# Kernel tuning notes

Measured on AMD Instinct MI355X. Metric: run time of the kernel, lower is better.

Reference implementation:

```python
import jax, jax.numpy as jnp
import numpy as np

MULTI_SCALE = [1, 3, 7, 9]
H = 8          # attention heads
EPS = 1e-8     # torch F.cosine_similarity eps


def _roi_avg_pool(feats_bct, rois, n_bins):
    """Temporal ROI adaptive average pooling (assumed behavior of `avr(i)`).
    feats_bct: [B, C, T]; rois: [N, 3] int (batch_idx, start, end) -> [N, C, n_bins].
    Bin b covers [s + floor(b*L/n), s + ceil((b+1)*L/n)) like adaptive_avg_pool1d.
    """
    T = feats_bct.shape[2]
    bidx, s, e = rois[:, 0], rois[:, 1], rois[:, 2]
    L = (e - s)[:, None, None]                               # [N,1,1]
    b = jnp.arange(n_bins, dtype=rois.dtype)[None, :, None]  # [1,nb,1]
    t = jnp.arange(T, dtype=rois.dtype)[None, None, :]       # [1,1,T]
    bs = s[:, None, None] + (b * L) // n_bins                # floor
    be = s[:, None, None] - (-(b + 1) * L) // n_bins         # ceil
    mask = ((t >= bs) & (t < be)).astype(feats_bct.dtype)    # [N,nb,T]
    mask = mask / jnp.clip(mask.sum(-1, keepdims=True), 1.0)
    roi_feats = feats_bct[bidx]                              # [N,C,T]
    return jnp.einsum('nit,nct->nci', mask, roi_feats)


def setup_inputs() -> dict:
    key = jax.random.key(0)
    ks = jax.random.split(key, 16)
    B, D, T, N = 4, 1024, 2048, 128
    hec = len(MULTI_SCALE)
    Cg = D // hec  # 256 channels per scale group
    inp = {
        'input_vectors': jax.random.normal(ks[0], (B, D, T), jnp.float32),
        'clstoken_scales': jax.random.normal(ks[1], (B, D), jnp.float32),
    }
    # rois: (batch_idx, start, end) with end > start
    bidx = jax.random.randint(ks[2], (N,), 0, B, jnp.int32)
    s = jax.random.randint(ks[3], (N,), 0, T // 2, jnp.int32)
    length = jax.random.randint(ks[4], (N,), 16, T // 2, jnp.int32)
    inp['rois'] = jnp.stack([bidx, s, jnp.minimum(s + length, T)], axis=1)
    sc = 1.0 / np.sqrt(D)
    inp['Wq'] = jax.random.normal(ks[5], (D, D), jnp.float32) * sc
    inp['bq'] = jnp.zeros((D,), jnp.float32)
    inp['Wk'] = jax.random.normal(ks[6], (D, D), jnp.float32) * sc
    inp['bk'] = jnp.zeros((D,), jnp.float32)
    inp['Wv'] = jax.random.normal(ks[7], (D, D), jnp.float32) * sc
    inp['bv'] = jnp.zeros((D,), jnp.float32)
    for j, nb in enumerate(MULTI_SCALE):
        csc = 1.0 / np.sqrt(Cg * nb)
        inp[f'conv_w{nb}'] = jax.random.normal(ks[8 + j], (Cg, Cg, nb), jnp.float32) * csc
        inp[f'conv_b{nb}'] = jnp.zeros((Cg,), jnp.float32)
    return inp


def reference(input_vectors, clstoken_scales, rois, Wq, bq, Wk, bk, Wv, bv,
              conv_w1, conv_b1, conv_w3, conv_b3, conv_w7, conv_b7, conv_w9, conv_b9):
    B, D, T = input_vectors.shape
    dk = D // H
    hec = len(MULTI_SCALE)
    x = input_vectors.transpose(0, 2, 1)                     # [B,T,D]
    # projections (torch Linear: y = x W^T + b)
    q = clstoken_scales @ Wq.T + bq                          # [B,D]
    k = (x @ Wk.T + bk).reshape(B, T, H, dk).transpose(0, 2, 1, 3)  # [B,H,T,dk]
    v = (x @ Wv.T + bv).reshape(B, T, H, dk).transpose(0, 2, 1, 3)  # [B,H,T,dk]
    qh = q.reshape(B, H, 1, dk)                              # [B,H,1,dk]
    # cosine-similarity pseudo-attention (no repeat blow-up: broadcast instead)
    dot = jnp.einsum('bhqd,bhtd->bht', qh, k)                # [B,H,T]
    nq = jnp.linalg.norm(qh, axis=-1)                        # [B,H,1]
    nk = jnp.linalg.norm(k, axis=-1)                         # [B,H,T]
    cos = dot / jnp.maximum(nq * nk, EPS)
    # eval mode: mask is all-ones, dropout identity
    p_attn = jnp.exp(jnp.abs(cos))                           # [B,H,T]
    val = p_attn[..., None] * v                              # [B,H,T,dk]
    # permute(0,1,3,2).view(B, hec, -1, T): group 2 heads per scale
    val = val.transpose(0, 1, 3, 2).reshape(B, hec, (H // hec) * dk, T)
    conv_ws = [conv_w1, conv_w3, conv_w7, conv_w9]
    conv_bs = [conv_b1, conv_b3, conv_b7, conv_b9]
    outs = []
    for j, nb in enumerate(MULTI_SCALE):
        pooled = _roi_avg_pool(val[:, j], rois, nb)          # [N, D//hec, nb]
        # Conv3d kernel (nb,1,1) stride (nb,1,1) on [N,C,nb,1,1] == full contraction
        outs.append(jnp.einsum('nci,oci->no', pooled, conv_ws[j]) + conv_bs[j])
    return jnp.concatenate(outs, axis=1)                     # [N_roi, D]
```

## Files before the change

kernel.cpp:

```cpp
#include <hip/hip_runtime.h>
#include <hip/hip_bf16.h>
#include <math.h>

#define BB   4
#define DD   1024
#define TT   2048
#define NH   8
#define DKH  128
#define NROI 128

typedef __attribute__((ext_vector_type(8))) __bf16 bf16x8;
typedef __attribute__((ext_vector_type(4))) float  f32x4;

#define OFF_Q    0
#define OFF_NQ   4096
#define OFF_KV   131072
#define OFF_POOL (131072 + 8388608)
#define POOL_FLOATS 655360
#define WS_F32_TOTAL (OFF_POOL + POOL_FLOATS)

__device__ __forceinline__ float bfu2f(unsigned short u) {
    return __uint_as_float(((unsigned int)u) << 16);
}

__global__ __launch_bounds__(256) void qproj_kernel(
    const float* __restrict__ cls, const float* __restrict__ Wq,
    const float* __restrict__ bq, float* __restrict__ q)
{
    const int blk  = blockIdx.x;
    const int b    = blk >> 8;
    const int dg   = blk & 255;
    const int warp = threadIdx.x >> 6;
    const int lane = threadIdx.x & 63;
    const int d    = dg * 4 + warp;
    const float* crow = cls + (size_t)b * DD;
    const float* wrow = Wq + (size_t)d * DD;
    float acc = 0.f;
    for (int i = lane; i < DD; i += 64) acc += crow[i] * wrow[i];
    #pragma unroll
    for (int off = 32; off; off >>= 1) acc += __shfl_down(acc, off);
    if (lane == 0) q[(size_t)b * DD + d] = acc + bq[d];
}

__global__ __launch_bounds__(64) void nq_kernel(
    const float* __restrict__ q, float* __restrict__ nq)
{
    const int bh = blockIdx.x;
    const int lane = threadIdx.x;
    const float* base = q + (size_t)bh * DKH;
    float v0 = base[lane], v1 = base[lane + 64];
    float acc = v0 * v0 + v1 * v1;
    #pragma unroll
    for (int off = 32; off; off >>= 1) acc += __shfl_down(acc, off);
    if (lane == 0) nq[bh] = sqrtf(acc);
}

__global__ __launch_bounds__(256) void convert_pair(
    const float* __restrict__ A, const float* __restrict__ B,
    __hip_bfloat16* __restrict__ Ab, __hip_bfloat16* __restrict__ Bb)
{
    const int i = blockIdx.x * 256 + threadIdx.x;
    float4 a = reinterpret_cast<const float4*>(A)[i];
    float4 b = reinterpret_cast<const float4*>(B)[i];
    union P4 { __hip_bfloat16 h[4]; ushort4 u; } pa, pb;
    pa.h[0] = __float2bfloat16(a.x); pa.h[1] = __float2bfloat16(a.y);
    pa.h[2] = __float2bfloat16(a.z); pa.h[3] = __float2bfloat16(a.w);
    pb.h[0] = __float2bfloat16(b.x); pb.h[1] = __float2bfloat16(b.y);
    pb.h[2] = __float2bfloat16(b.z); pb.h[3] = __float2bfloat16(b.w);
    reinterpret_cast<ushort4*>(Ab)[i] = pa.u;
    reinterpret_cast<ushort4*>(Bb)[i] = pb.u;
}

__global__ __launch_bounds__(256) void transpose_convert(
    const float* __restrict__ X, __hip_bfloat16* __restrict__ Xt)
{
    __shared__ float tile[64][65];
    const int t0 = blockIdx.x * 64, d0 = blockIdx.y * 64, b = blockIdx.z;
    const int tid = threadIdx.x;
    const int g = tid >> 6, tl = tid & 63;
    const float* src = X + ((size_t)(b * DD + d0)) * TT + t0;
    #pragma unroll
    for (int i = 0; i < 16; ++i)
        tile[g * 16 + i][tl] = src[(size_t)(g * 16 + i) * TT + tl];
    __syncthreads();
    const int lane = tid & 63, w = tid >> 6;
    const int dq = (lane & 15) * 4;
    const int th = lane >> 4;
    __hip_bfloat16* dst = Xt + ((size_t)(b * TT + t0)) * DD + d0;
    #pragma unroll
    for (int i = 0; i < 4; ++i) {
        const int t = w * 4 + th + i * 16;
        union { __hip_bfloat16 h[4]; ushort4 u; } P;
        P.h[0] = __float2bfloat16(tile[dq + 0][t]);
        P.h[1] = __float2bfloat16(tile[dq + 1][t]);
        P.h[2] = __float2bfloat16(tile[dq + 2][t]);
        P.h[3] = __float2bfloat16(tile[dq + 3][t]);
        *reinterpret_cast<ushort4*>(&dst[(size_t)t * DD + dq]) = P.u;
    }
}

__device__ __forceinline__ void glds16(const __hip_bfloat16* g, __hip_bfloat16* l)
{
    __builtin_amdgcn_global_load_lds(
        (const __attribute__((address_space(1))) void*)g,
        (__attribute__((address_space(3))) void*)l, 16, 0, 0);
}

__global__ __launch_bounds__(512) void fused_kv(
    const __hip_bfloat16* __restrict__ Wkb,
    const __hip_bfloat16* __restrict__ Wvb,
    const __hip_bfloat16* __restrict__ Xt,
    const float* __restrict__ bk, const float* __restrict__ bv,
    const float* __restrict__ q,  const float* __restrict__ nq,
    __hip_bfloat16* __restrict__ val)
{
    const int t0 = blockIdx.x * 128;
    const int m0 = blockIdx.y * 128;
    const int b  = blockIdx.z;

    __shared__ __hip_bfloat16 AsK[128 * 32];
    __shared__ __hip_bfloat16 AsV[128 * 32];
    __shared__ __hip_bfloat16 Bs[128 * 32];
    __shared__ float qs[128];
    __shared__ float rdot[2][128];
    __shared__ float rsq[2][128];
    __shared__ float p_lds[128];

    const int tid  = threadIdx.x;
    const int lane = tid & 63;
    const int w    = tid >> 6;
    const int wr   = w >> 2;
    const int wc   = w & 3;

    if (tid < 128) qs[tid] = q[(size_t)b * DD + m0 + tid];

    const int st_row = tid >> 2;
    const int st_g   = (tid & 3) ^ ((st_row >> 1) & 3);

    const __hip_bfloat16* WkS = Wkb + (size_t)(m0 + st_row) * DD + st_g * 8;
    const __hip_bfloat16* WvS = Wvb + (size_t)(m0 + st_row) * DD + st_g * 8;
    const __hip_bfloat16* XS  = Xt + ((size_t)(b * TT + t0 + st_row)) * DD + st_g * 8;
    __hip_bfloat16* K0 = AsK + (w * 16) * 32;
    __hip_bfloat16* V0 = AsV + (w * 16) * 32;
    __hip_bfloat16* B0 = Bs  + (w * 16) * 32;

    f32x4 ak[4][2], av[4][2];
    #pragma unroll
    for (int i = 0; i < 4; ++i)
        #pragma unroll
        for (int j = 0; j < 2; ++j) {
            ak[i][j] = (f32x4){0.f, 0.f, 0.f, 0.f};
            av[i][j] = (f32x4){0.f, 0.f, 0.f, 0.f};
        }

    for (int k0 = 0; k0 < DD; k0 += 32) {
        glds16(WkS + k0, K0);
        glds16(WvS + k0, V0);
        glds16(XS  + k0, B0);
        __syncthreads();

        const int g = lane >> 4;
        bf16x8 bfx[2], afk[4], afv[4];
        #pragma unroll
        for (int fn = 0; fn < 2; ++fn) {
            const int r = wc * 32 + fn * 16 + (lane & 15);
            const int s = g ^ ((r >> 1) & 3);
            bfx[fn] = *reinterpret_cast<const bf16x8*>(&Bs[r * 32 + s * 8]);
        }
        #pragma unroll
        for (int fm = 0; fm < 4; ++fm) {
            const int r = wr * 64 + fm * 16 + (lane & 15);
            const int s = g ^ ((r >> 1) & 3);
            afk[fm] = *reinterpret_cast<const bf16x8*>(&AsK[r * 32 + s * 8]);
            afv[fm] = *reinterpret_cast<const bf16x8*>(&AsV[r * 32 + s * 8]);
        }
        #pragma unroll
        for (int fm = 0; fm < 4; ++fm)
            #pragma unroll
            for (int fn = 0; fn < 2; ++fn)
                ak[fm][fn] = __builtin_amdgcn_mfma_f32_16x16x32_bf16(
                    afk[fm], bfx[fn], ak[fm][fn], 0, 0, 0);
        #pragma unroll
        for (int fm = 0; fm < 4; ++fm)
            #pragma unroll
            for (int fn = 0; fn < 2; ++fn)
                av[fm][fn] = __builtin_amdgcn_mfma_f32_16x16x32_bf16(
                    afv[fm], bfx[fn], av[fm][fn], 0, 0, 0);
        __syncthreads();
    }

    const int lg = lane >> 4;
    #pragma unroll
    for (int fn = 0; fn < 2; ++fn) {
        float dp = 0.f, sp = 0.f;
        #pragma unroll
        for (int fm = 0; fm < 4; ++fm) {
            const int mb = wr * 64 + fm * 16 + lg * 4;
            #pragma unroll
            for (int r = 0; r < 4; ++r) {
                const float kv = ak[fm][fn][r] + bk[m0 + mb + r];
                dp += kv * qs[mb + r];
                sp += kv * kv;
            }
        }
        dp += __shfl_xor(dp, 16); sp += __shfl_xor(sp, 16);
        dp += __shfl_xor(dp, 32); sp += __shfl_xor(sp, 32);
        if (lane < 16) {
            rdot[wr][wc * 32 + fn * 16 + lane] = dp;
            rsq[wr][wc * 32 + fn * 16 + lane]  = sp;
        }
    }
    __syncthreads();
    if (tid < 128) {
        const float dd = rdot[0][tid] + rdot[1][tid];
        const float ss = rsq[0][tid] + rsq[1][tid];
        const int head = m0 >> 7;
        const float c = dd / fmaxf(nq[b * NH + head] * sqrtf(ss), 1e-8f);
        p_lds[tid] = expf(fabsf(c));
    }
    __syncthreads();

    float pv[2];
    #pragma unroll
    for (int fn = 0; fn < 2; ++fn)
        pv[fn] = p_lds[wc * 32 + fn * 16 + (lane & 15)];

    const int tbase = t0 + wc * 32 + (lane & 15);
    #pragma unroll
    for (int fm = 0; fm < 4; ++fm) {
        const int m = m0 + wr * 64 + fm * 16 + lg * 4;
        const float4 b4 = *reinterpret_cast<const float4*>(&bv[m]);
        #pragma unroll
        for (int fn = 0; fn < 2; ++fn) {
            const int t = tbase + fn * 16;
            const f32x4 a = av[fm][fn];
            const float pf = pv[fn];
            union { __hip_bfloat16 h[4]; ushort4 u; } P;
            P.h[0] = __float2bfloat16((a[0] + b4.x) * pf);
            P.h[1] = __float2bfloat16((a[1] + b4.y) * pf);
            P.h[2] = __float2bfloat16((a[2] + b4.z) * pf);
            P.h[3] = __float2bfloat16((a[3] + b4.w) * pf);
            *reinterpret_cast<ushort4*>(&val[((size_t)(b * TT + t)) * DD + m]) = P.u;
        }
    }
}

#define POOL_WAVES 16
__global__ __launch_bounds__(1024) void pool_kernel(
    const __hip_bfloat16* __restrict__ val, const int* __restrict__ rois,
    float* __restrict__ pooled)
{
    const int n    = blockIdx.x;
    const int sc   = blockIdx.y;
    const int tid  = threadIdx.x;
    const int lane = tid & 63;
    const int w    = tid >> 6;

    const int nbt[4]  = {1, 3, 7, 9};
    const int offt[4] = {0, 32768, 131072, 360448};
    const int nb  = nbt[sc];
    const int off = offt[sc];

    __shared__ float lacc[9][256];
    for (int i = tid; i < nb * 256; i += 1024)
        ((float*)lacc)[i] = 0.f;

    const int bidx = rois[n * 3 + 0];
    const int s    = rois[n * 3 + 1];
    const int e    = rois[n * 3 + 2];
    const int L    = e - s;
    __syncthreads();

    const int ts = s + (w * L) / POOL_WAVES;
    const int te = s + ((w + 1) * L) / POOL_WAVES;

    const int cq = lane * 4;
    const __hip_bfloat16* vb = val + (size_t)bidx * TT * DD + sc * 256 + cq;

    if (te > ts) {
        int bin = ((ts - s) * nb) / L;
        int nbs = s + ((bin + 1) * L) / nb;
        int cbe = s + ((bin + 1) * L + nb - 1) / nb;

        if (bin > 0 && ts < s + (bin * L + nb - 1) / nb) {
            const ushort4 u = *reinterpret_cast<const ushort4*>(&vb[(size_t)ts * DD]);
            atomicAdd(&lacc[bin - 1][cq + 0], bfu2f(u.x));
            atomicAdd(&lacc[bin - 1][cq + 1], bfu2f(u.y));
            atomicAdd(&lacc[bin - 1][cq + 2], bfu2f(u.z));
            atomicAdd(&lacc[bin - 1][cq + 3], bfu2f(u.w));
        }

        float a0 = 0.f, a1 = 0.f, a2 = 0.f, a3 = 0.f;
        int t = ts;
        while (true) {
            const int seg = min(te, nbs);
            for (; t + 4 <= seg; t += 4) {
                const ushort4 u0 = *reinterpret_cast<const ushort4*>(&vb[(size_t)(t    ) * DD]);
                const ushort4 u1 = *reinterpret_cast<const ushort4*>(&vb[(size_t)(t + 1) * DD]);
                const ushort4 u2 = *reinterpret_cast<const ushort4*>(&vb[(size_t)(t + 2) * DD]);
                const ushort4 u3 = *reinterpret_cast<const ushort4*>(&vb[(size_t)(t + 3) * DD]);
                a0 += bfu2f(u0.x) + bfu2f(u1.x) + bfu2f(u2.x) + bfu2f(u3.x);
                a1 += bfu2f(u0.y) + bfu2f(u1.y) + bfu2f(u2.y) + bfu2f(u3.y);
                a2 += bfu2f(u0.z) + bfu2f(u1.z) + bfu2f(u2.z) + bfu2f(u3.z);
                a3 += bfu2f(u0.w) + bfu2f(u1.w) + bfu2f(u2.w) + bfu2f(u3.w);
            }
            for (; t < seg; ++t) {
                const ushort4 u = *reinterpret_cast<const ushort4*>(&vb[(size_t)t * DD]);
                a0 += bfu2f(u.x); a1 += bfu2f(u.y);
                a2 += bfu2f(u.z); a3 += bfu2f(u.w);
            }
            if (t >= te) break;
            const ushort4 u = *reinterpret_cast<const ushort4*>(&vb[(size_t)t * DD]);
            const float v0 = bfu2f(u.x), v1 = bfu2f(u.y),
                        v2 = bfu2f(u.z), v3 = bfu2f(u.w);
            if (t < cbe) { a0 += v0; a1 += v1; a2 += v2; a3 += v3; }
            atomicAdd(&lacc[bin][cq + 0], a0);
            atomicAdd(&lacc[bin][cq + 1], a1);
            atomicAdd(&lacc[bin][cq + 2], a2);
            atomicAdd(&lacc[bin][cq + 3], a3);
            a0 = v0; a1 = v1; a2 = v2; a3 = v3;
            ++bin; ++t;
            nbs = s + ((bin + 1) * L) / nb;
            cbe = s + ((bin + 1) * L + nb - 1) / nb;
        }
        atomicAdd(&lacc[bin][cq + 0], a0);
        atomicAdd(&lacc[bin][cq + 1], a1);
        atomicAdd(&lacc[bin][cq + 2], a2);
        atomicAdd(&lacc[bin][cq + 3], a3);
    }
    __syncthreads();

    float* po = pooled + off + (size_t)n * 256 * nb;
    for (int i = tid; i < nb * 256; i += 1024) {
        const int bin = i >> 8, ch = i & 255;
        const int bs  = s + (bin * L) / nb;
        const int be  = s + ((bin + 1) * L + nb - 1) / nb;
        po[(size_t)ch * nb + bin] = lacc[bin][ch] / (float)max(be - bs, 1);
    }
}

__global__ __launch_bounds__(256) void out_gemm(
    const float* __restrict__ pooled,
    const float* __restrict__ w1, const float* __restrict__ b1,
    const float* __restrict__ w3, const float* __restrict__ b3,
    const float* __restrict__ w7, const float* __restrict__ b7,
    const float* __restrict__ w9, const float* __restrict__ b9,
    float* __restrict__ out)
{
    const int z = blockIdx.z;
    int sc, kc;
    if      (z == 0)  { sc = 0; kc = 0; }
    else if (z < 4)   { sc = 1; kc = z - 1; }
    else if (z < 11)  { sc = 2; kc = z - 4; }
    else              { sc = 3; kc = z - 11; }

    int nb, off; const float* W; const float* bias;
    switch (sc) {
        case 0:  nb = 1; off = 0;      W = w1; bias = b1; break;
        case 1:  nb = 3; off = 32768;  W = w3; bias = b3; break;
        case 2:  nb = 7; off = 131072; W = w7; bias = b7; break;
        default: nb = 9; off = 360448; W = w9; bias = b9; break;
    }
    const int Kj = 256 * nb;
    const float* P = pooled + off;

    const int o0 = blockIdx.x * 32;
    const int n0 = blockIdx.y * 32;
    const int kbase = kc * 256;

    __shared__ float Ps[32][33];
    __shared__ float Ws[32][33];

    const int tid = threadIdx.x;
    const int tx = tid & 15, ty = tid >> 4;
    float acc[2][2] = {};

    for (int k0 = kbase; k0 < kbase + 256; k0 += 32) {
        #pragma unroll
        for (int i = 0; i < 4; ++i) {
            const int li = tid + i * 256;
            const int r = li >> 5, k = li & 31;
            Ps[r][k] = P[(size_t)(n0 + r) * Kj + k0 + k];
            Ws[r][k] = W[(size_t)(o0 + r) * Kj + k0 + k];
        }
        __syncthreads();
        #pragma unroll
        for (int k = 0; k < 32; ++k) {
            const float p0 = Ps[ty][k],  p1 = Ps[ty + 16][k];
            const float w0 = Ws[tx][k],  w1v = Ws[tx + 16][k];
            acc[0][0] = fmaf(p0, w0,  acc[0][0]);
            acc[0][1] = fmaf(p0, w1v, acc[0][1]);
            acc[1][0] = fmaf(p1, w0,  acc[1][0]);
            acc[1][1] = fmaf(p1, w1v, acc[1][1]);
        }
        __syncthreads();
    }
    #pragma unroll
    for (int i = 0; i < 2; ++i) {
        const int n = n0 + ty + 16 * i;
        #pragma unroll
        for (int jj = 0; jj < 2; ++jj) {
            const int o = o0 + tx + 16 * jj;
            const float add = (kc == 0) ? bias[o] : 0.f;
            atomicAdd(&out[(size_t)n * DD + sc * 256 + o], acc[i][jj] + add);
        }
    }
}

extern "C" void kernel_launch(void* const* d_in, const int* in_sizes, int n_in,
                              void* d_out, int out_size, void* d_ws, size_t ws_size,
                              hipStream_t stream)
{
    const float* inp  = (const float*)d_in[0];
    const float* cls  = (const float*)d_in[1];
    const int*   rois = (const int*)  d_in[2];
    const float* Wq   = (const float*)d_in[3];
    const float* bq   = (const float*)d_in[4];
    const float* Wk   = (const float*)d_in[5];
    const float* bk   = (const float*)d_in[6];
    const float* Wv   = (const float*)d_in[7];
    const float* bv   = (const float*)d_in[8];
    const float* cw1  = (const float*)d_in[9];  const float* cb1 = (const float*)d_in[10];
    const float* cw3  = (const float*)d_in[11]; const float* cb3 = (const float*)d_in[12];
    const float* cw7  = (const float*)d_in[13]; const float* cb7 = (const float*)d_in[14];
    const float* cw9  = (const float*)d_in[15]; const float* cb9 = (const float*)d_in[16];

    float* out = (float*)d_out;
    float* ws  = (float*)d_ws;
    float* q      = ws + OFF_Q;
    float* nq     = ws + OFF_NQ;
    __hip_bfloat16* val = (__hip_bfloat16*)(ws + OFF_KV);
    float* pooled = ws + OFF_POOL;
    __hip_bfloat16* bfb = (__hip_bfloat16*)(ws + WS_F32_TOTAL);
    __hip_bfloat16* Wkb = bfb;
    __hip_bfloat16* Wvb = bfb + 1048576;
    __hip_bfloat16* Xt  = bfb + 2097152;

    convert_pair<<<dim3(1024), 256, 0, stream>>>(Wk, Wv, Wkb, Wvb);
    transpose_convert<<<dim3(TT / 64, DD / 64, BB), 256, 0, stream>>>(inp, Xt);
    qproj_kernel<<<dim3(BB * 256), 256, 0, stream>>>(cls, Wq, bq, q);
    nq_kernel<<<dim3(BB * NH), 64, 0, stream>>>(q, nq);
    fused_kv<<<dim3(TT / 128, DD / 128, BB), 512, 0, stream>>>(
        Wkb, Wvb, Xt, bk, bv, q, nq, val);
    pool_kernel<<<dim3(NROI, 4), 1024, 0, stream>>>(val, rois, pooled);
    hipMemsetAsync(out, 0, (size_t)out_size * sizeof(float), stream);
    out_gemm<<<dim3(8, 4, 20), 256, 0, stream>>>(pooled, cw1, cb1, cw3, cb3,
                                                 cw7, cb7, cw9, cb9, out);
}
```

Baseline: 114.0 us.

## Double-buffer LDS in fused KV GEMM, fold q-norm in, vectorize transpose loads

```diff
diff --git a/kernel.cpp b/kernel.cpp
--- a/kernel.cpp
+++ b/kernel.cpp
@@ -13,7 +13,6 @@
 typedef __attribute__((ext_vector_type(4))) float  f32x4;
 
 #define OFF_Q    0
-#define OFF_NQ   4096
 #define OFF_KV   131072
 #define OFF_POOL (131072 + 8388608)
 #define POOL_FLOATS 655360
@@ -42,19 +41,6 @@
     if (lane == 0) q[(size_t)b * DD + d] = acc + bq[d];
 }
 
-__global__ __launch_bounds__(64) void nq_kernel(
-    const float* __restrict__ q, float* __restrict__ nq)
-{
-    const int bh = blockIdx.x;
-    const int lane = threadIdx.x;
-    const float* base = q + (size_t)bh * DKH;
-    float v0 = base[lane], v1 = base[lane + 64];
-    float acc = v0 * v0 + v1 * v1;
-    #pragma unroll
-    for (int off = 32; off; off >>= 1) acc += __shfl_down(acc, off);
-    if (lane == 0) nq[bh] = sqrtf(acc);
-}
-
 __global__ __launch_bounds__(256) void convert_pair(
     const float* __restrict__ A, const float* __restrict__ B,
     __hip_bfloat16* __restrict__ Ab, __hip_bfloat16* __restrict__ Bb)
@@ -77,11 +63,18 @@
     __shared__ float tile[64][65];
     const int t0 = blockIdx.x * 64, d0 = blockIdx.y * 64, b = blockIdx.z;
     const int tid = threadIdx.x;
-    const int g = tid >> 6, tl = tid & 63;
     const float* src = X + ((size_t)(b * DD + d0)) * TT + t0;
-    #pragma unroll
-    for (int i = 0; i < 16; ++i)
-        tile[g * 16 + i][tl] = src[(size_t)(g * 16 + i) * TT + tl];
+    const int f4c = tid & 15;
+    const int r0  = tid >> 4;
+    #pragma unroll
+    for (int i = 0; i < 4; ++i) {
+        const int r = r0 + 16 * i;
+        const float4 v = *reinterpret_cast<const float4*>(&src[(size_t)r * TT + f4c * 4]);
+        tile[r][f4c * 4 + 0] = v.x;
+        tile[r][f4c * 4 + 1] = v.y;
+        tile[r][f4c * 4 + 2] = v.z;
+        tile[r][f4c * 4 + 3] = v.w;
+    }
     __syncthreads();
     const int lane = tid & 63, w = tid >> 6;
     const int dq = (lane & 15) * 4;
@@ -111,16 +104,16 @@
     const __hip_bfloat16* __restrict__ Wvb,
     const __hip_bfloat16* __restrict__ Xt,
     const float* __restrict__ bk, const float* __restrict__ bv,
-    const float* __restrict__ q,  const float* __restrict__ nq,
+    const float* __restrict__ q,
     __hip_bfloat16* __restrict__ val)
 {
     const int t0 = blockIdx.x * 128;
     const int m0 = blockIdx.y * 128;
     const int b  = blockIdx.z;
 
-    __shared__ __hip_bfloat16 AsK[128 * 32];
-    __shared__ __hip_bfloat16 AsV[128 * 32];
-    __shared__ __hip_bfloat16 Bs[128 * 32];
+    __shared__ __hip_bfloat16 AsK[2][128 * 32];
+    __shared__ __hip_bfloat16 AsV[2][128 * 32];
+    __shared__ __hip_bfloat16 Bs[2][128 * 32];
     __shared__ float qs[128];
     __shared__ float rdot[2][128];
     __shared__ float rsq[2][128];
@@ -140,9 +133,7 @@
     const __hip_bfloat16* WkS = Wkb + (size_t)(m0 + st_row) * DD + st_g * 8;
     const __hip_bfloat16* WvS = Wvb + (size_t)(m0 + st_row) * DD + st_g * 8;
     const __hip_bfloat16* XS  = Xt + ((size_t)(b * TT + t0 + st_row)) * DD + st_g * 8;
-    __hip_bfloat16* K0 = AsK + (w * 16) * 32;
-    __hip_bfloat16* V0 = AsV + (w * 16) * 32;
-    __hip_bfloat16* B0 = Bs  + (w * 16) * 32;
+    const int ldsoff = (w * 16) * 32;
 
     f32x4 ak[4][2], av[4][2];
     #pragma unroll
@@ -153,26 +144,27 @@
             av[i][j] = (f32x4){0.f, 0.f, 0.f, 0.f};
         }
 
-    for (int k0 = 0; k0 < DD; k0 += 32) {
-        glds16(WkS + k0, K0);
-        glds16(WvS + k0, V0);
-        glds16(XS  + k0, B0);
-        __syncthreads();
-
+    auto STAGE = [&](int buf, int k0) {
+        glds16(WkS + k0, AsK[buf] + ldsoff);
+        glds16(WvS + k0, AsV[buf] + ldsoff);
+        glds16(XS  + k0, Bs[buf]  + ldsoff);
+    };
+
+    auto COMPUTE = [&](int buf) {
         const int g = lane >> 4;
         bf16x8 bfx[2], afk[4], afv[4];
         #pragma unroll
         for (int fn = 0; fn < 2; ++fn) {
             const int r = wc * 32 + fn * 16 + (lane & 15);
             const int s = g ^ ((r >> 1) & 3);
-            bfx[fn] = *reinterpret_cast<const bf16x8*>(&Bs[r * 32 + s * 8]);
+            bfx[fn] = *reinterpret_cast<const bf16x8*>(&Bs[buf][r * 32 + s * 8]);
         }
         #pragma unroll
         for (int fm = 0; fm < 4; ++fm) {
             const int r = wr * 64 + fm * 16 + (lane & 15);
             const int s = g ^ ((r >> 1) & 3);
-            afk[fm] = *reinterpret_cast<const bf16x8*>(&AsK[r * 32 + s * 8]);
-            afv[fm] = *reinterpret_cast<const bf16x8*>(&AsV[r * 32 + s * 8]);
+            afk[fm] = *reinterpret_cast<const bf16x8*>(&AsK[buf][r * 32 + s * 8]);
+            afv[fm] = *reinterpret_cast<const bf16x8*>(&AsV[buf][r * 32 + s * 8]);
         }
         #pragma unroll
         for (int fm = 0; fm < 4; ++fm)
@@ -186,8 +178,18 @@
             for (int fn = 0; fn < 2; ++fn)
                 av[fm][fn] = __builtin_amdgcn_mfma_f32_16x16x32_bf16(
                     afv[fm], bfx[fn], av[fm][fn], 0, 0, 0);
+    };
+
+    int cur = 0;
+    STAGE(0, 0);
+    __syncthreads();
+    for (int k0 = 32; k0 < DD; k0 += 32) {
+        STAGE(cur ^ 1, k0);
+        COMPUTE(cur);
         __syncthreads();
-    }
+        cur ^= 1;
+    }
+    COMPUTE(cur);
 
     const int lg = lane >> 4;
     #pragma unroll
@@ -214,8 +216,9 @@
     if (tid < 128) {
         const float dd = rdot[0][tid] + rdot[1][tid];
         const float ss = rsq[0][tid] + rsq[1][tid];
-        const int head = m0 >> 7;
-        const float c = dd / fmaxf(nq[b * NH + head] * sqrtf(ss), 1e-8f);
+        float qn2 = 0.f;
+        for (int j = 0; j < 128; ++j) qn2 += qs[j] * qs[j];
+        const float c = dd / fmaxf(sqrtf(qn2) * sqrtf(ss), 1e-8f);
         p_lds[tid] = expf(fabsf(c));
     }
     __syncthreads();
@@ -428,7 +431,6 @@
     float* out = (float*)d_out;
     float* ws  = (float*)d_ws;
     float* q      = ws + OFF_Q;
-    float* nq     = ws + OFF_NQ;
     __hip_bfloat16* val = (__hip_bfloat16*)(ws + OFF_KV);
     float* pooled = ws + OFF_POOL;
     __hip_bfloat16* bfb = (__hip_bfloat16*)(ws + WS_F32_TOTAL);
@@ -439,9 +441,8 @@
     convert_pair<<<dim3(1024), 256, 0, stream>>>(Wk, Wv, Wkb, Wvb);
     transpose_convert<<<dim3(TT / 64, DD / 64, BB), 256, 0, stream>>>(inp, Xt);
     qproj_kernel<<<dim3(BB * 256), 256, 0, stream>>>(cls, Wq, bq, q);
-    nq_kernel<<<dim3(BB * NH), 64, 0, stream>>>(q, nq);
     fused_kv<<<dim3(TT / 128, DD / 128, BB), 512, 0, stream>>>(
-        Wkb, Wvb, Xt, bk, bv, q, nq, val);
+        Wkb, Wvb, Xt, bk, bv, q, val);
     pool_kernel<<<dim3(NROI, 4), 1024, 0, stream>>>(val, rois, pooled);
     hipMemsetAsync(out, 0, (size_t)out_size * sizeof(float), stream);
     out_gemm<<<dim3(8, 4, 20), 256, 0, stream>>>(pooled, cw1, cb1, cw3, cb3,
```

Result: no change. 113.5 us (-0.4%).
